# Kernel tuning notes

Hardware: AMD Instinct MI355X
Metric: run time of the kernel (lower is better)

The kernel has to match this reference:

```python
import jax, jax.numpy as jnp
import numpy as np

# Dimensions: decode-style paged attention with INT4 + Hamming(8,4) SECDED ECC
B, Q, S, H, KVH, D = 8, 16, 4096, 32, 8, 128
BLOCK_SIZE = 16
BLOCKS_PER_SEQ = S // BLOCK_SIZE      # 256
NUM_BLOCKS = B * BLOCKS_PER_SEQ       # 2048


def _bit(x, i):
    return (x >> i) & 1


def hamming84_encode(nib):
    """Encode 4-bit nibbles (int32 in [0,16)) into Hamming(8,4) SECDED codewords.
    Bit layout (0-indexed): [p1, p2, d1, p4, d2, d3, d4, overall_parity]."""
    d1, d2, d3, d4 = _bit(nib, 0), _bit(nib, 1), _bit(nib, 2), _bit(nib, 3)
    p1 = d1 ^ d2 ^ d4
    p2 = d1 ^ d3 ^ d4
    p4 = d2 ^ d3 ^ d4
    cw7 = p1 | (p2 << 1) | (d1 << 2) | (p4 << 3) | (d2 << 4) | (d3 << 5) | (d4 << 6)
    par = p1 ^ p2 ^ d1 ^ p4 ^ d2 ^ d3 ^ d4
    return cw7 | (par << 7)


def hamming84_decode(cw):
    """Syndrome decode: correct single-bit errors (syndrome!=0, overall parity odd),
    detect-but-pass-through double errors. Returns the 4-bit nibble."""
    b = [_bit(cw, i) for i in range(8)]
    s1 = b[0] ^ b[2] ^ b[4] ^ b[6]
    s2 = b[1] ^ b[2] ^ b[5] ^ b[6]
    s4 = b[3] ^ b[4] ^ b[5] ^ b[6]
    syn = s1 + 2 * s2 + 4 * s4
    overall = b[0] ^ b[1] ^ b[2] ^ b[3] ^ b[4] ^ b[5] ^ b[6] ^ b[7]
    flip = jnp.where((syn > 0) & (overall == 1),
                     jnp.left_shift(jnp.int32(1), jnp.maximum(syn - 1, 0)),
                     jnp.int32(0))
    cwc = cw ^ flip
    return _bit(cwc, 2) | (_bit(cwc, 4) << 1) | (_bit(cwc, 5) << 2) | (_bit(cwc, 6) << 3)


def quantize_int4(x):
    """Symmetric per-token per-head INT4 quant: scale = absmax/7, nibble in [0,16)."""
    scale = jnp.maximum(jnp.max(jnp.abs(x), axis=-1) / 7.0, 1e-8)  # [B,S,KVH]
    nib = jnp.clip(jnp.round(x / scale[..., None]), -8, 7).astype(jnp.int32) + 8
    return nib, scale


def write_and_read(x, block_table):
    """Quantize -> Hamming84 encode -> scatter into paged cache via block table,
    then gather -> decode -> dequantize. x: [B,S,KVH,D] float."""
    nib, scale = quantize_int4(x)
    cw = hamming84_encode(nib)
    bt = block_table.reshape(-1)                                   # [B*BLOCKS_PER_SEQ]
    cw_blocks = cw.reshape(B * BLOCKS_PER_SEQ, BLOCK_SIZE, KVH, D)
    sc_blocks = scale.reshape(B * BLOCKS_PER_SEQ, BLOCK_SIZE, KVH)
    cache = jnp.zeros((NUM_BLOCKS, BLOCK_SIZE, KVH, D), dtype=jnp.int32).at[bt].set(cw_blocks)
    scales = jnp.zeros((NUM_BLOCKS, BLOCK_SIZE, KVH), dtype=x.dtype).at[bt].set(sc_blocks)
    g_cw = cache[bt].reshape(B, S, KVH, D)
    g_sc = scales[bt].reshape(B, S, KVH)
    nib_dec = hamming84_decode(g_cw)
    return (nib_dec.astype(x.dtype) - 8.0) * g_sc[..., None]


def setup_inputs() -> dict:
    key = jax.random.key(0)
    kq, kk, kv = jax.random.split(key, 3)
    q = jax.random.normal(kq, (B, Q, H, D), dtype=jnp.float32)
    k = jax.random.normal(kk, (B, S, KVH, D), dtype=jnp.float32)
    v = jax.random.normal(kv, (B, S, KVH, D), dtype=jnp.float32)
    block_table = jnp.arange(NUM_BLOCKS, dtype=jnp.int32).reshape(B, BLOCKS_PER_SEQ)
    return {"q": q, "k": k, "v": v, "block_table": block_table}


def reference(q, k, v, block_table):
    k_d = write_and_read(k, block_table)   # [B,S,KVH,D] dequantized keys
    v_d = write_and_read(v, block_table)
    G = H // KVH
    qg = q.reshape(B, Q, KVH, G, D)
    scores = jnp.einsum('bqhgd,bshd->bhgqs', qg, k_d) / jnp.sqrt(jnp.float32(D))
    # queries are the last Q positions of the S-token context (causal)
    qpos = S - Q + jnp.arange(Q)
    kpos = jnp.arange(S)
    mask = kpos[None, :] <= qpos[:, None]                          # [Q,S]
    scores = jnp.where(mask[None, None, None], scores, jnp.float32(-1e30))
    attn = jax.nn.softmax(scores, axis=-1)
    out = jnp.einsum('bhgqs,bshd->bqhgd', attn, v_d)
    return out.reshape(B, Q, H, D)
```

## Files before the change

### kernel.cpp

```cpp
#include <hip/hip_runtime.h>
#include <hip/hip_bf16.h>

#define B_    8
#define Qn    16
#define S_    4096
#define Hh    32
#define KVH_  8
#define D_    128
#define G_    4
#define ROWS  64
#define KT    32
#define NT_TOT (S_ / KT)
#define NCHUNK 12
#define THREADS 256
#define VTS   40

typedef unsigned int u32;
typedef unsigned short u16;
typedef __attribute__((ext_vector_type(8))) short short8;
typedef __attribute__((ext_vector_type(4))) float f32x4;

__device__ __forceinline__ u16 f2bf(float f){
  union{u32 u; float f;} t; t.f = f; u32 u = t.u;
  return (u16)((u + 0x7fffu + ((u >> 16) & 1u)) >> 16);
}
__device__ __forceinline__ float bf2f(u16 h){
  union{u32 x; float f;} t; t.x = ((u32)h) << 16; return t.f;
}
__device__ __forceinline__ u16 qnib(float x, float inv){
  union{float f; u32 u;} t; t.f = rintf(x * inv);
  return (u16)(t.u >> 16);
}

__device__ __forceinline__ void gll16(const float* g, const void* lds){
  __builtin_amdgcn_global_load_lds((const __attribute__((address_space(1))) void*)g,
                                   (__attribute__((address_space(3))) void*)lds,
                                   16, 0, 0);
}
#define SBAR0 __builtin_amdgcn_sched_barrier(0)

__global__ __launch_bounds__(THREADS)
__attribute__((amdgpu_waves_per_eu(3)))
void attn_partial(const float* __restrict__ q, const float* __restrict__ k,
                  const float* __restrict__ v, float* __restrict__ part_o,
                  float* __restrict__ part_ml)
{
  __shared__ __attribute__((aligned(16))) float rawK[KT * D_];
  __shared__ __attribute__((aligned(16))) float rawV[KT * D_];
  __shared__ u16   kn[KT * D_];
  __shared__ u16   vt[D_ * VTS];
  __shared__ float ksc[KT];
  __shared__ float vsc[KT];

  const int kvh   = blockIdx.x;
  const int chunk = blockIdx.y;
  const int b     = blockIdx.z;
  const int tid   = threadIdx.x;
  const int lane  = tid & 63;
  const int w     = tid >> 6;
  const int l15   = lane & 15;
  const int l4    = lane >> 4;
  const int t0    = (chunk * NT_TOT) / NCHUNK;
  const int t1    = ((chunk + 1) * NT_TOT) / NCHUNK;
  const float RS = 0.08838834764831844f;

  const int lt  = tid >> 3;
  const int qd4 = (tid & 7) * 4;

  short8 qhi[4], qlo[4];
  {
    const int h = kvh * G_ + w;
    const float* qp = q + (((size_t)(b * Qn + l15) * Hh) + h) * (size_t)D_ + (l4 * 8);
    #pragma unroll
    for (int kc = 0; kc < 4; ++kc){
      const float4 a = *(const float4*)(qp + kc * 32);
      const float4 c = *(const float4*)(qp + kc * 32 + 4);
      const float fv[8] = {a.x, a.y, a.z, a.w, c.x, c.y, c.z, c.w};
      #pragma unroll
      for (int i = 0; i < 8; ++i){
        const u16 hi = f2bf(fv[i]);
        qhi[kc][i] = (short)hi;
        qlo[kc][i] = (short)f2bf(fv[i] - bf2f(hi));
      }
    }
  }

  float m_i = -1e30f, l_i = 0.f;
  f32x4 acc_o[8];
  #pragma unroll
  for (int df = 0; df < 8; ++df) acc_o[df] = (f32x4)0.f;

  const int lhi = lane >> 5, cp = lane & 31;
  int goff[4];
  #pragma unroll
  for (int j = 0; j < 4; ++j){
    const int tokp = (w * 4 + j) * 2 + lhi;
    goff[j] = tokp * (KVH_ * D_) + (cp << 2);
  }
  const size_t tb0 = ((size_t)b * S_) * KVH_ * D_ + (size_t)kvh * D_;
  const char* rawKb = (const char*)rawK;
  const char* rawVb = (const char*)rawV;

  {
    const size_t base = tb0 + (size_t)(t0 * KT) * KVH_ * D_;
    #pragma unroll
    for (int j = 0; j < 4; ++j) gll16(k + base + goff[j], rawKb + (w * 4 + j) * 1024);
    #pragma unroll
    for (int j = 0; j < 4; ++j) gll16(v + base + goff[j], rawVb + (w * 4 + j) * 1024);
  }

  for (int t = t0; t < t1; ++t){
    const int s0 = t * KT;
    const int sn = (s0 + KT <= S_ - KT) ? (s0 + KT) : (S_ - KT);
    const size_t base_n = tb0 + (size_t)sn * KVH_ * D_;

    __builtin_amdgcn_s_barrier();
    SBAR0;

    asm volatile("s_waitcnt vmcnt(4)" ::: "memory"); SBAR0;
    float4 kr[4];
    #pragma unroll
    for (int m = 0; m < 4; ++m)
      kr[m] = *(const float4*)(rawK + lt * D_ + qd4 + m * 32);
    asm volatile("s_waitcnt lgkmcnt(0)" ::: "memory"); SBAR0;

    #pragma unroll
    for (int j = 0; j < 4; ++j) gll16(k + base_n + goff[j], rawKb + (w * 4 + j) * 1024);
    SBAR0;

    {
      float am = 0.f;
      #pragma unroll
      for (int m = 0; m < 4; ++m)
        am = fmaxf(am, fmaxf(fmaxf(fabsf(kr[m].x), fabsf(kr[m].y)),
                             fmaxf(fabsf(kr[m].z), fabsf(kr[m].w))));
      am = fmaxf(am, __shfl_xor(am, 1));
      am = fmaxf(am, __shfl_xor(am, 2));
      am = fmaxf(am, __shfl_xor(am, 4));
      const float sc = fmaxf(am * (1.f / 7.f), 1e-8f);
      if ((tid & 7) == 0) ksc[lt] = sc;
      const float inv = 1.f / sc;
      #pragma unroll
      for (int m = 0; m < 4; ++m){
        const int d0 = qd4 + m * 32;
        const int idx = lt * D_ + ((((d0 >> 3) ^ (lt & 7)) << 3) | (d0 & 7));
        *(ushort4*)&kn[idx] = make_ushort4(qnib(kr[m].x, inv), qnib(kr[m].y, inv),
                                           qnib(kr[m].z, inv), qnib(kr[m].w, inv));
      }
    }

    asm volatile("s_waitcnt vmcnt(4)" ::: "memory"); SBAR0;
    float4 vr[4];
    #pragma unroll
    for (int m = 0; m < 4; ++m)
      vr[m] = *(const float4*)(rawV + lt * D_ + qd4 + m * 32);
    asm volatile("s_waitcnt lgkmcnt(0)" ::: "memory"); SBAR0;

    #pragma unroll
    for (int j = 0; j < 4; ++j) gll16(v + base_n + goff[j], rawVb + (w * 4 + j) * 1024);
    SBAR0;

    {
      float am = 0.f;
      #pragma unroll
      for (int m = 0; m < 4; ++m)
        am = fmaxf(am, fmaxf(fmaxf(fabsf(vr[m].x), fabsf(vr[m].y)),
                             fmaxf(fabsf(vr[m].z), fabsf(vr[m].w))));
      am = fmaxf(am, __shfl_xor(am, 1));
      am = fmaxf(am, __shfl_xor(am, 2));
      am = fmaxf(am, __shfl_xor(am, 4));
      const float sc = fmaxf(am * (1.f / 7.f), 1e-8f);
      if ((tid & 7) == 0) vsc[lt] = sc;
      const float inv = 1.f / sc;
      #pragma unroll
      for (int m = 0; m < 4; ++m){
        const int d0 = qd4 + m * 32;
        vt[(d0 + 0) * VTS + lt] = qnib(vr[m].x, inv);
        vt[(d0 + 1) * VTS + lt] = qnib(vr[m].y, inv);
        vt[(d0 + 2) * VTS + lt] = qnib(vr[m].z, inv);
        vt[(d0 + 3) * VTS + lt] = qnib(vr[m].w, inv);
      }
    }
    asm volatile("s_waitcnt lgkmcnt(0)" ::: "memory"); SBAR0;
    __builtin_amdgcn_s_barrier();
    SBAR0;

    f32x4 st[2];
    st[0] = (f32x4)0.f; st[1] = (f32x4)0.f;
    __builtin_amdgcn_s_setprio(1);
    #pragma unroll
    for (int kc = 0; kc < 4; ++kc){
      #pragma unroll
      for (int cf = 0; cf < 2; ++cf){
        const int tok = cf * 16 + l15;
        const int gr  = kc * 4 + l4;
        const short8 kf = *(const short8*)&kn[tok * D_ + ((gr ^ (tok & 7)) << 3)];
        st[cf] = __builtin_amdgcn_mfma_f32_16x16x32_bf16(kf, qhi[kc], st[cf], 0, 0, 0);
        st[cf] = __builtin_amdgcn_mfma_f32_16x16x32_bf16(kf, qlo[kc], st[cf], 0, 0, 0);
      }
    }
    __builtin_amdgcn_s_setprio(0);

    float ksr[2][4], vsv[2][4];
    #pragma unroll
    for (int cf = 0; cf < 2; ++cf){
      const float4 ks = *(const float4*)&ksc[cf * 16 + l4 * 4];
      const float4 vs = *(const float4*)&vsc[cf * 16 + l4 * 4];
      ksr[cf][0] = ks.x * RS; ksr[cf][1] = ks.y * RS;
      ksr[cf][2] = ks.z * RS; ksr[cf][3] = ks.w * RS;
      vsv[cf][0] = vs.x; vsv[cf][1] = vs.y; vsv[cf][2] = vs.z; vsv[cf][3] = vs.w;
    }
    const bool need_mask = (s0 + KT > S_ - Qn);
    float x[2][4]; float rm = -1e30f;
    #pragma unroll
    for (int cf = 0; cf < 2; ++cf)
      #pragma unroll
      for (int r = 0; r < 4; ++r){
        float xx = st[cf][r] * ksr[cf][r];
        if (need_mask && (s0 + cf * 16 + l4 * 4 + r > S_ - Qn + l15)) xx = -1e30f;
        x[cf][r] = xx; rm = fmaxf(rm, xx);
      }
    rm = fmaxf(rm, __shfl_xor(rm, 16));
    rm = fmaxf(rm, __shfl_xor(rm, 32));
    const float mn  = fmaxf(m_i, rm);
    const float fac = __expf(m_i - mn);
    m_i = mn;
    float p[2][4]; float rs = 0.f;
    #pragma unroll
    for (int cf = 0; cf < 2; ++cf)
      #pragma unroll
      for (int r = 0; r < 4; ++r){
        p[cf][r] = __expf(x[cf][r] - mn);
        rs += p[cf][r];
      }
    rs += __shfl_xor(rs, 16);
    rs += __shfl_xor(rs, 32);
    l_i = l_i * fac + rs;

    u32 pk0[2], pk1[2];
    #pragma unroll
    for (int rp = 0; rp < 2; ++rp){
      pk0[rp] = (u32)f2bf(p[0][2*rp] * vsv[0][2*rp]) | ((u32)f2bf(p[0][2*rp+1] * vsv[0][2*rp+1]) << 16);
      pk1[rp] = (u32)f2bf(p[1][2*rp] * vsv[1][2*rp]) | ((u32)f2bf(p[1][2*rp+1] * vsv[1][2*rp+1]) << 16);
    }
    const int s0L = ((l4 & 1) * 2) * 16 + l15;
    const int s1L = s0L + 16;
    const u32 a00 = __shfl((int)pk0[0], s0L), a01 = __shfl((int)pk0[1], s0L);
    const u32 a02 = __shfl((int)pk0[0], s1L), a03 = __shfl((int)pk0[1], s1L);
    const u32 a10 = __shfl((int)pk1[0], s0L), a11 = __shfl((int)pk1[1], s0L);
    const u32 a12 = __shfl((int)pk1[0], s1L), a13 = __shfl((int)pk1[1], s1L);
    const bool hi = (l4 >= 2);
    union { uint4 u; short8 s; } pfu;
    pfu.u = make_uint4(hi ? a10 : a00, hi ? a11 : a01,
                       hi ? a12 : a02, hi ? a13 : a03);
    const short8 pf = pfu.s;

    f32x4 facv;
    #pragma unroll
    for (int r = 0; r < 4; ++r) facv[r] = __shfl(fac, l4 * 4 + r);
    #pragma unroll
    for (int df = 0; df < 8; ++df) acc_o[df] *= facv;

    __builtin_amdgcn_s_setprio(1);
    #pragma unroll
    for (int df = 0; df < 8; ++df){
      const int d = df * 16 + l15;
      const short8 vf = *(const short8*)&vt[d * VTS + l4 * 8];
      acc_o[df] = __builtin_amdgcn_mfma_f32_16x16x32_bf16(pf, vf, acc_o[df], 0, 0, 0);
    }
    __builtin_amdgcn_s_setprio(0);
  }

  asm volatile("s_waitcnt vmcnt(0)" ::: "memory"); SBAR0;

  {
    const size_t base = (((size_t)b * KVH_ + kvh) * (size_t)NCHUNK + chunk) * ROWS;
    #pragma unroll
    for (int r = 0; r < 4; ++r){
      const int qrow = (w << 4) + (l4 << 2) + r;
      #pragma unroll
      for (int df = 0; df < 8; ++df)
        part_o[(base + qrow) * D_ + df * 16 + l15] = acc_o[df][r];
    }
    if (l4 == 0){
      part_ml[(base + (w << 4) + l15) * 2 + 0] = m_i;
      part_ml[(base + (w << 4) + l15) * 2 + 1] = l_i;
    }
  }
}

__global__ void attn_reduce(const float* __restrict__ part_o, const float* __restrict__ part_ml,
                            float* __restrict__ out)
{
  const int row = blockIdx.x;
  const int kvh = blockIdx.y;
  const int b   = blockIdx.z;
  const int d   = threadIdx.x;
  const size_t base = ((size_t)b * KVH_ + kvh) * (size_t)NCHUNK;

  float M = -1e30f;
  for (int c = 0; c < NCHUNK; ++c)
    M = fmaxf(M, part_ml[((base + c) * ROWS + row) * 2 + 0]);
  float acc = 0.f, lt = 0.f;
  #pragma unroll
  for (int c = 0; c < NCHUNK; ++c){
    const float m = part_ml[((base + c) * ROWS + row) * 2 + 0];
    const float l = part_ml[((base + c) * ROWS + row) * 2 + 1];
    const float w = __expf(m - M);
    lt += w * l;
    acc += w * part_o[((base + c) * ROWS + row) * D_ + d];
  }
  const int g = row >> 4, qi = row & 15;
  out[(((size_t)b * Qn + qi) * Hh + kvh * G_ + g) * (size_t)D_ + d] = acc / lt;
}

extern "C" void kernel_launch(void* const* d_in, const int* in_sizes, int n_in,
                              void* d_out, int out_size, void* d_ws, size_t ws_size,
                              hipStream_t stream)
{
  const float* q = (const float*)d_in[0];
  const float* k = (const float*)d_in[1];
  const float* v = (const float*)d_in[2];
  float* out = (float*)d_out;

  float* part_o  = (float*)d_ws;
  float* part_ml = part_o + (size_t)B_ * KVH_ * NCHUNK * ROWS * D_;

  attn_partial<<<dim3(KVH_, NCHUNK, B_), THREADS, 0, stream>>>(q, k, v, part_o, part_ml);
  attn_reduce<<<dim3(ROWS, KVH_, B_), 128, 0, stream>>>(part_o, part_ml, out);
}
```

Baseline: 63.65 us.

## Fuse split-K reduction into partial kernel via last-block atomic counter

Removes the separate reduce kernel launch. Each block increments a per-(batch, kv-head) atomic counter after writing its partials, and the last block to arrive merges all chunks with vectorized float4 loads. The change also skips the redundant prefetch on each block's final tile and waits for outstanding loads inside the loop instead of after it. It adds a memset launch, threadfence/atomic synchronization, and a serial tail on the last block of each group.

```diff
diff --git a/kernel.cpp b/kernel.cpp
--- a/kernel.cpp
+++ b/kernel.cpp
@@ -43,7 +43,8 @@
 __attribute__((amdgpu_waves_per_eu(3)))
 void attn_partial(const float* __restrict__ q, const float* __restrict__ k,
                   const float* __restrict__ v, float* __restrict__ part_o,
-                  float* __restrict__ part_ml)
+                  float* __restrict__ part_ml, int* __restrict__ cnt,
+                  float* __restrict__ out)
 {
   __shared__ __attribute__((aligned(16))) float rawK[KT * D_];
   __shared__ __attribute__((aligned(16))) float rawV[KT * D_];
@@ -51,6 +52,7 @@
   __shared__ u16   vt[D_ * VTS];
   __shared__ float ksc[KT];
   __shared__ float vsc[KT];
+  __shared__ int   lastflag;
 
   const int kvh   = blockIdx.x;
   const int chunk = blockIdx.y;
@@ -111,8 +113,8 @@
 
   for (int t = t0; t < t1; ++t){
     const int s0 = t * KT;
-    const int sn = (s0 + KT <= S_ - KT) ? (s0 + KT) : (S_ - KT);
-    const size_t base_n = tb0 + (size_t)sn * KVH_ * D_;
+    const bool last = (t == t1 - 1);
+    const size_t base_n = tb0 + (size_t)(s0 + KT) * KVH_ * D_;
 
     __builtin_amdgcn_s_barrier();
     SBAR0;
@@ -124,8 +126,10 @@
       kr[m] = *(const float4*)(rawK + lt * D_ + qd4 + m * 32);
     asm volatile("s_waitcnt lgkmcnt(0)" ::: "memory"); SBAR0;
 
-    #pragma unroll
-    for (int j = 0; j < 4; ++j) gll16(k + base_n + goff[j], rawKb + (w * 4 + j) * 1024);
+    if (!last){
+      #pragma unroll
+      for (int j = 0; j < 4; ++j) gll16(k + base_n + goff[j], rawKb + (w * 4 + j) * 1024);
+    }
     SBAR0;
 
     {
@@ -149,15 +153,19 @@
       }
     }
 
-    asm volatile("s_waitcnt vmcnt(4)" ::: "memory"); SBAR0;
+    if (!last){ asm volatile("s_waitcnt vmcnt(4)" ::: "memory"); }
+    else      { asm volatile("s_waitcnt vmcnt(0)" ::: "memory"); }
+    SBAR0;
     float4 vr[4];
     #pragma unroll
     for (int m = 0; m < 4; ++m)
       vr[m] = *(const float4*)(rawV + lt * D_ + qd4 + m * 32);
     asm volatile("s_waitcnt lgkmcnt(0)" ::: "memory"); SBAR0;
 
-    #pragma unroll
-    for (int j = 0; j < 4; ++j) gll16(v + base_n + goff[j], rawVb + (w * 4 + j) * 1024);
+    if (!last){
+      #pragma unroll
+      for (int j = 0; j < 4; ++j) gll16(v + base_n + goff[j], rawVb + (w * 4 + j) * 1024);
+    }
     SBAR0;
 
     {
@@ -271,8 +279,6 @@
     __builtin_amdgcn_s_setprio(0);
   }
 
-  asm volatile("s_waitcnt vmcnt(0)" ::: "memory"); SBAR0;
-
   {
     const size_t base = (((size_t)b * KVH_ + kvh) * (size_t)NCHUNK + chunk) * ROWS;
     #pragma unroll
@@ -287,31 +293,54 @@
       part_ml[(base + (w << 4) + l15) * 2 + 1] = l_i;
     }
   }
-}
-
-__global__ void attn_reduce(const float* __restrict__ part_o, const float* __restrict__ part_ml,
-                            float* __restrict__ out)
-{
-  const int row = blockIdx.x;
-  const int kvh = blockIdx.y;
-  const int b   = blockIdx.z;
-  const int d   = threadIdx.x;
-  const size_t base = ((size_t)b * KVH_ + kvh) * (size_t)NCHUNK;
-
-  float M = -1e30f;
-  for (int c = 0; c < NCHUNK; ++c)
-    M = fmaxf(M, part_ml[((base + c) * ROWS + row) * 2 + 0]);
-  float acc = 0.f, lt = 0.f;
-  #pragma unroll
-  for (int c = 0; c < NCHUNK; ++c){
-    const float m = part_ml[((base + c) * ROWS + row) * 2 + 0];
-    const float l = part_ml[((base + c) * ROWS + row) * 2 + 1];
-    const float w = __expf(m - M);
-    lt += w * l;
-    acc += w * part_o[((base + c) * ROWS + row) * D_ + d];
-  }
-  const int g = row >> 4, qi = row & 15;
-  out[(((size_t)b * Qn + qi) * Hh + kvh * G_ + g) * (size_t)D_ + d] = acc / lt;
+
+  __syncthreads();
+  if (tid == 0){
+    __threadfence();
+    const int old = __hip_atomic_fetch_add(&cnt[b * KVH_ + kvh], 1,
+                                           __ATOMIC_ACQ_REL,
+                                           __HIP_MEMORY_SCOPE_AGENT);
+    lastflag = (old == NCHUNK - 1);
+  }
+  __syncthreads();
+  if (lastflag){
+    __threadfence();
+    const size_t rbase = ((size_t)b * KVH_ + kvh) * (size_t)NCHUNK;
+    const int row  = tid >> 2;
+    const int dseg = (tid & 3) * 32;
+    float M = -1e30f;
+    #pragma unroll 4
+    for (int c = 0; c < NCHUNK; ++c)
+      M = fmaxf(M, part_ml[((rbase + c) * ROWS + row) * 2 + 0]);
+    f32x4 acc[8];
+    #pragma unroll
+    for (int j = 0; j < 8; ++j) acc[j] = (f32x4)0.f;
+    float lt_sum = 0.f;
+    for (int c = 0; c < NCHUNK; ++c){
+      const size_t ri = (rbase + c) * ROWS + row;
+      const float mm = part_ml[ri * 2 + 0];
+      const float ll = part_ml[ri * 2 + 1];
+      const float wt = __expf(mm - M);
+      lt_sum += wt * ll;
+      const float* src = part_o + ri * D_ + dseg;
+      #pragma unroll
+      for (int j = 0; j < 8; ++j){
+        const float4 pv = *(const float4*)(src + j * 4);
+        acc[j][0] += wt * pv.x; acc[j][1] += wt * pv.y;
+        acc[j][2] += wt * pv.z; acc[j][3] += wt * pv.w;
+      }
+    }
+    const float invl = 1.f / lt_sum;
+    const int g = row >> 4, qi = row & 15;
+    float* dst = out + (((size_t)b * Qn + qi) * Hh + kvh * G_ + g) * (size_t)D_ + dseg;
+    #pragma unroll
+    for (int j = 0; j < 8; ++j){
+      float4 o4;
+      o4.x = acc[j][0] * invl; o4.y = acc[j][1] * invl;
+      o4.z = acc[j][2] * invl; o4.w = acc[j][3] * invl;
+      *(float4*)(dst + j * 4) = o4;
+    }
+  }
 }
 
 extern "C" void kernel_launch(void* const* d_in, const int* in_sizes, int n_in,
@@ -325,7 +354,10 @@
 
   float* part_o  = (float*)d_ws;
   float* part_ml = part_o + (size_t)B_ * KVH_ * NCHUNK * ROWS * D_;
-
-  attn_partial<<<dim3(KVH_, NCHUNK, B_), THREADS, 0, stream>>>(q, k, v, part_o, part_ml);
-  attn_reduce<<<dim3(ROWS, KVH_, B_), 128, 0, stream>>>(part_o, part_ml, out);
-}
+  int*   cnt     = (int*)(part_ml + (size_t)B_ * KVH_ * NCHUNK * ROWS * 2);
+
+  hipMemsetAsync(cnt, 0, B_ * KVH_ * sizeof(int), stream);
+
+  attn_partial<<<dim3(KVH_, NCHUNK, B_), THREADS, 0, stream>>>(
+      q, k, v, part_o, part_ml, cnt, out);
+}
```

New measurement: 168.0 us. 164% more time.
